# Kernel optimization log

Measured on AMD Instinct MI355X. Metric: run time of the kernel, lower is better.

The kernel has to match this reference:

```python
import jax, jax.numpy as jnp
import numpy as np

N = 50000    # nodes
E = 800000   # edges per relation
R = 3        # relations
IN, HID, OUT = 128, 128, 64


def setup_inputs() -> dict:
    key = jax.random.key(0)
    ks = jax.random.split(key, 7)
    x = jax.random.normal(ks[0], (N, IN), jnp.float32)
    src = jax.random.randint(ks[1], (R, E), 0, N)
    dst = jax.random.randint(ks[2], (R, E), 0, N)
    W1 = jax.random.normal(ks[3], (R, IN, HID), jnp.float32) / np.sqrt(IN)
    b1 = jnp.zeros((R, HID), jnp.float32)
    W2 = jax.random.normal(ks[4], (R, HID, OUT), jnp.float32) / np.sqrt(HID)
    b2 = jnp.zeros((R, OUT), jnp.float32)
    return {"x": x, "src": src, "dst": dst, "W1": W1, "b1": b1, "W2": W2, "b2": b2}


def _rel_conv(x, src, dst, W, b):
    """dgl GraphConv with norm='both' and self-loops added (dgl.add_self_loop).
    out = D_dst^{-1/2} A_sl (D_src^{-1/2} X W) + b  (weight order commutes)."""
    loop = jnp.arange(N, dtype=src.dtype)
    s = jnp.concatenate([src, loop])  # [E+N] self-loops appended
    d = jnp.concatenate([dst, loop])
    ones = jnp.ones(s.shape[0], x.dtype)
    deg_out = jax.ops.segment_sum(ones, s, num_segments=N)  # >= 1 due to self loops
    deg_in = jax.ops.segment_sum(ones, d, num_segments=N)
    h = (x * jax.lax.rsqrt(deg_out)[:, None]) @ W          # [N, F_out]
    agg = jax.ops.segment_sum(h[s], d, num_segments=N)     # gather-scatter SpMM
    return agg * jax.lax.rsqrt(deg_in)[:, None] + b


def _hetero_layer(x, src, dst, W, b):
    # HeteroGraphConv with aggregate='sum': sum per-relation GraphConv outputs.
    out = _rel_conv(x, src[0], dst[0], W[0], b[0])
    for r in range(1, R):  # small fixed relation count
        out = out + _rel_conv(x, src[r], dst[r], W[r], b[r])
    return out


def reference(x, src, dst, W1, b1, W2, b2):
    h = jax.nn.relu(_hetero_layer(x, src, dst, W1, b1))
    return _hetero_layer(h, src, dst, W2, b2)
```

## Files before the change

### kernel.cpp

```cpp
#include <hip/hip_runtime.h>
#include <hip/hip_fp16.h>


constexpr int N   = 50000;
constexpr int R   = 3;
constexpr int IN  = 128;
constexpr int HID = 128;
constexpr int OUT = 64;
constexpr int M   = R * N;
constexpr int BK  = 1024;
constexpr int NBKT = (M + BK - 1) / BK;
constexpr int CHUNK = 8192;
constexpr int KB  = 24;
constexpr int CVT_N4 = N * IN / 4;
constexpr int WPK   = 6 * KB * 64;
constexpr int WPK_B = (WPK + 255) / 256;

typedef _Float16 half8 __attribute__((ext_vector_type(8)));
typedef float floatx16 __attribute__((ext_vector_type(16)));

__global__ void prep_kernel(const float* __restrict__ x,
                            const float* __restrict__ W1, const float* __restrict__ W2,
                            const float* __restrict__ b1, const float* __restrict__ b2,
                            uint2* __restrict__ x16,
                            __half* __restrict__ F1, __half* __restrict__ F2,
                            float* __restrict__ bsum1, float* __restrict__ bsum2) {
    int b = blockIdx.x;
    if (b == 0) {
        int t = threadIdx.x;
        if (t < HID) bsum1[t] = b1[t] + b1[HID + t] + b1[2 * HID + t];
        if (t < OUT) bsum2[t] = b2[t] + b2[OUT + t] + b2[2 * OUT + t];
        return;
    }
    if (b <= WPK_B) {
        int idx = (b - 1) * 256 + threadIdx.x;
        if (idx < 4 * KB * 64) {
            int nt = idx / (KB * 64), rem = idx % (KB * 64);
            int kb = rem / 64, lane = rem % 64;
            int c = nt * 32 + (lane & 31);
            int k0 = kb * 16 + (lane >> 5) * 8;
            __half h[8];
#pragma unroll
            for (int j = 0; j < 8; j++) h[j] = __float2half_rn(W1[(k0 + j) * 128 + c]);
            *(uint4*)(F1 + (size_t)idx * 8) = *(uint4*)h;
        } else if (idx < 6 * KB * 64) {
            int i2 = idx - 4 * KB * 64;
            int nt = i2 / (KB * 64), rem = i2 % (KB * 64);
            int kb = rem / 64, lane = rem % 64;
            int c = nt * 32 + (lane & 31);
            int k0 = kb * 16 + (lane >> 5) * 8;
            __half h[8];
#pragma unroll
            for (int j = 0; j < 8; j++) h[j] = __float2half_rn(W2[(k0 + j) * 64 + c]);
            *(uint4*)(F2 + (size_t)i2 * 8) = *(uint4*)h;
        }
        return;
    }
    int i = (b - 1 - WPK_B) * 256 + threadIdx.x;
    if (i >= CVT_N4) return;
    float4 v = ((const float4*)x)[i];
    __half2 a = __floats2half2_rn(v.x, v.y);
    __half2 c = __floats2half2_rn(v.z, v.w);
    uint2 o;
    o.x = *(unsigned*)&a;
    o.y = *(unsigned*)&c;
    x16[i] = o;
}

__global__ __launch_bounds__(256) void p1_kernel(const int* __restrict__ src,
                                                 const int* __restrict__ dst,
                                                 int E, int RE, int nb,
                                                 int* __restrict__ bh) {
    __shared__ int hd[NBKT], hs[NBKT];
    for (int i = threadIdx.x; i < NBKT; i += 256) { hd[i] = 0; hs[i] = 0; }
    __syncthreads();
    int beg = blockIdx.x * CHUNK, end = min(RE, beg + CHUNK);
    for (int g = beg + (int)threadIdx.x; g < end; g += 256) {
        int rb = ((g >= E) + (g >= 2 * E)) * N;
        atomicAdd(&hd[(rb + dst[g]) >> 10], 1);
        atomicAdd(&hs[(rb + src[g]) >> 10], 1);
    }
    __syncthreads();
    for (int i = threadIdx.x; i < NBKT; i += 256) {
        bh[i * nb + blockIdx.x] = hd[i];
        bh[(NBKT + i) * nb + blockIdx.x] = hs[i];
    }
}

__global__ void scan1_kernel(const int* __restrict__ in, int* __restrict__ out,
                             int* __restrict__ partials, int L) {
    __shared__ int lds[1024];
    int t = threadIdx.x;
    int idx = blockIdx.x * 1024 + t;
    int v = (idx < L) ? in[idx] : 0;
    lds[t] = v;
    __syncthreads();
    for (int off = 1; off < 1024; off <<= 1) {
        int u = (t >= off) ? lds[t - off] : 0;
        __syncthreads();
        lds[t] += u;
        __syncthreads();
    }
    if (idx < L) out[idx] = lds[t] - v;
    if (t == 1023) partials[blockIdx.x] = lds[1023];
}

__global__ void scan2_kernel(int* __restrict__ partials, int nb1) {
    __shared__ int lds[256];
    int t = threadIdx.x;
    int v = (t < nb1) ? partials[t] : 0;
    lds[t] = v;
    __syncthreads();
    for (int off = 1; off < 256; off <<= 1) {
        int u = (t >= off) ? lds[t - off] : 0;
        __syncthreads();
        lds[t] += u;
        __syncthreads();
    }
    if (t < nb1) partials[t] = lds[t] - v;
}

__global__ __launch_bounds__(256) void p3_kernel(const int* __restrict__ src,
                                                 const int* __restrict__ dst,
                                                 int E, int RE, int nb,
                                                 const int* __restrict__ scanv,
                                                 const int* __restrict__ partials,
                                                 int* __restrict__ ebd,
                                                 unsigned short* __restrict__ ebs) {
    __shared__ int cd[NBKT], cs[NBKT];
    for (int i = threadIdx.x; i < NBKT; i += 256) {
        int id = i * nb + blockIdx.x;
        int is = (NBKT + i) * nb + blockIdx.x;
        cd[i] = scanv[id] + partials[id >> 10];
        cs[i] = scanv[is] + partials[is >> 10] - RE;
    }
    __syncthreads();
    int beg = blockIdx.x * CHUNK, end = min(RE, beg + CHUNK);
    for (int g = beg + (int)threadIdx.x; g < end; g += 256) {
        int rb = ((g >= E) + (g >= 2 * E)) * N;
        int s  = src[g];
        int kd = rb + dst[g];
        int pd = atomicAdd(&cd[kd >> 10], 1);
        ebd[pd] = (s << 10) | (kd & 1023);
        int ks = rb + s;
        int ps = atomicAdd(&cs[ks >> 10], 1);
        ebs[ps] = (unsigned short)(ks & 1023);
    }
}

__global__ __launch_bounds__(1024) void pbs_kernel(const int* __restrict__ scanv,
                                                   const int* __restrict__ partials,
                                                   int nb, int RE,
                                                   const unsigned short* __restrict__ ebs,
                                                   float* __restrict__ rs_out) {
    __shared__ int cnt[BK];
    int t = threadIdx.x;
    int k = blockIdx.x;
    int i0 = (NBKT + k) * nb;
    int segbeg = scanv[i0] + partials[i0 >> 10] - RE;
    int segend;
    if (k == NBKT - 1) segend = RE;
    else {
        int i1 = i0 + nb;
        segend = scanv[i1] + partials[i1 >> 10] - RE;
    }
    cnt[t] = 0;
    __syncthreads();
    for (int e = segbeg + t; e < segend; e += 1024)
        atomicAdd(&cnt[(int)ebs[e]], 1);
    __syncthreads();
    int slot = k * BK + t;
    if (slot < M) rs_out[slot] = rsqrtf((float)(cnt[t] + 1));
}

__global__ __launch_bounds__(1024) void pbd_kernel(const int* __restrict__ scanv,
                                                   const int* __restrict__ partials,
                                                   int nb, int RE,
                                                   const int* __restrict__ ebd,
                                                   const float* __restrict__ rs_out,
                                                   int* __restrict__ row_ptr,
                                                   float* __restrict__ rs_in,
                                                   unsigned int* __restrict__ esrc) {
    __shared__ int cnt[BK];
    __shared__ int cur[BK];
    int t = threadIdx.x;
    int k = blockIdx.x;
    int i0 = k * nb;
    int segbeg = scanv[i0] + partials[i0 >> 10];
    int segend;
    if (k == NBKT - 1) segend = RE;
    else {
        int i1 = (k + 1) * nb;
        segend = scanv[i1] + partials[i1 >> 10];
    }
    cnt[t] = 0;
    __syncthreads();
    for (int e = segbeg + t; e < segend; e += 1024)
        atomicAdd(&cnt[ebd[e] & 1023], 1);
    __syncthreads();
    int slot = k * BK + t;
    int c = cnt[t];
    cur[t] = c;
    __syncthreads();
    for (int off = 1; off < 1024; off <<= 1) {
        int u = (t >= off) ? cur[t - off] : 0;
        __syncthreads();
        cur[t] += u;
        __syncthreads();
    }
    int excl = cur[t] - c;
    if (slot < M) {
        row_ptr[slot] = segbeg + excl;
        rs_in[slot] = rsqrtf((float)(c + 1));
    }
    if (k == NBKT - 1 && t == 0) row_ptr[M] = RE;
    __syncthreads();
    cur[t] = segbeg + excl;
    __syncthreads();
    for (int e = segbeg + t; e < segend; e += 1024) {
        int v = ebd[e];
        int key = k * BK + (v & 1023);
        int r = (key >= 2 * N) + (key >= N);
        unsigned s = (unsigned)(v >> 10);
        int pos = atomicAdd(&cur[v & 1023], 1);
        __half h = __float2half_rn(rs_out[r * N + s]);
        esrc[pos] = s | ((unsigned)__half_as_ushort(h) << 16);
    }
}

__global__ __launch_bounds__(256) void gather_kernel(const __half* __restrict__ Xh,
                                                     const float* __restrict__ rs_in,
                                                     const float* __restrict__ rs_out,
                                                     const int* __restrict__ row_ptr,
                                                     const unsigned int* __restrict__ esrc,
                                                     __half* __restrict__ Z16) {
    int n = blockIdx.x * 4 + (threadIdx.x >> 6);
    if (n >= N) return;
    int lane = threadIdx.x & 63;
    int g = lane >> 4;
    int cl = lane & 15;
    const __half* xrow = Xh + (long)n * 128 + cl * 8;
    uint4 xn = *(const uint4*)xrow;
#pragma unroll
    for (int r = 0; r < R; r++) {
        int key = r * N + n;
        int beg = row_ptr[key], end = row_ptr[key + 1];
        __half2 a0 = __float2half2_rn(0.f), a1 = a0, a2 = a0, a3 = a0;
        for (int e = beg; e < end; e += 24) {
            unsigned u[6];
#pragma unroll
            for (int j = 0; j < 6; j++) {
                int idx = e + 4 * j + g;
                u[j] = (idx < end) ? esrc[idx] : 0u;
            }
            uint4 y[6];
#pragma unroll
            for (int j = 0; j < 6; j++)
                y[j] = *(const uint4*)(Xh + (long)(u[j] & 0xffffu) * 128 + cl * 8);
#pragma unroll
            for (int j = 0; j < 6; j++) {
                __half2 cj = __half2half2(__ushort_as_half((unsigned short)(u[j] >> 16)));
                a0 = __hfma2(*(__half2*)&y[j].x, cj, a0);
                a1 = __hfma2(*(__half2*)&y[j].y, cj, a1);
                a2 = __hfma2(*(__half2*)&y[j].z, cj, a2);
                a3 = __hfma2(*(__half2*)&y[j].w, cj, a3);
            }
        }
#pragma unroll
        for (int off = 16; off < 64; off <<= 1) {
            unsigned w0 = *(unsigned*)&a0, w1 = *(unsigned*)&a1;
            unsigned w2 = *(unsigned*)&a2, w3 = *(unsigned*)&a3;
            unsigned v0 = (unsigned)__shfl_xor((int)w0, off, 64);
            unsigned v1 = (unsigned)__shfl_xor((int)w1, off, 64);
            unsigned v2 = (unsigned)__shfl_xor((int)w2, off, 64);
            unsigned v3 = (unsigned)__shfl_xor((int)w3, off, 64);
            a0 = __hadd2(a0, *(__half2*)&v0);
            a1 = __hadd2(a1, *(__half2*)&v1);
            a2 = __hadd2(a2, *(__half2*)&v2);
            a3 = __hadd2(a3, *(__half2*)&v3);
        }
        __half2 cs = __float2half2_rn(rs_out[key]);
        a0 = __hfma2(*(__half2*)&xn.x, cs, a0);
        a1 = __hfma2(*(__half2*)&xn.y, cs, a1);
        a2 = __hfma2(*(__half2*)&xn.z, cs, a2);
        a3 = __hfma2(*(__half2*)&xn.w, cs, a3);
        __half2 ri = __float2half2_rn(rs_in[key]);
        a0 = __hmul2(a0, ri);
        a1 = __hmul2(a1, ri);
        a2 = __hmul2(a2, ri);
        a3 = __hmul2(a3, ri);
        if (g == 0) {
            uint4 o;
            o.x = *(unsigned*)&a0;
            o.y = *(unsigned*)&a1;
            o.z = *(unsigned*)&a2;
            o.w = *(unsigned*)&a3;
            *(uint4*)(Z16 + (long)n * 384 + r * 128 + cl * 8) = o;
        }
    }
}

__global__ __launch_bounds__(256) void mfma_gemm1_kernel(const __half* __restrict__ Z16,
                                                         const __half* __restrict__ F,
                                                         const float* __restrict__ bias,
                                                         __half* __restrict__ H16) {
    int wave = threadIdx.x >> 6, lane = threadIdx.x & 63;
    int m0 = blockIdx.x * 128 + wave * 32;
    int mr = min(m0 + (lane & 31), N - 1);
    const half8* A = (const half8*)(Z16 + (long)mr * 384 + (lane >> 5) * 8);
    const half8* B = (const half8*)F;
    floatx16 acc[4];
#pragma unroll
    for (int i = 0; i < 4; i++)
#pragma unroll
        for (int j = 0; j < 16; j++) acc[i][j] = 0.f;

    half8 a = A[0];
    for (int kb = 0; kb < KB; kb++) {
        half8 an = (kb < KB - 1) ? A[(kb + 1) * 2] : a;
#pragma unroll
        for (int nt = 0; nt < 4; nt++) {
            half8 b = B[(nt * KB + kb) * 64 + lane];
            acc[nt] = __builtin_amdgcn_mfma_f32_32x32x16_f16(a, b, acc[nt], 0, 0, 0);
        }
        a = an;
    }
    float bv[4];
#pragma unroll
    for (int nt = 0; nt < 4; nt++) bv[nt] = bias[nt * 32 + (lane & 31)];
    int rbase = m0 + 4 * (lane >> 5);
    int col0 = lane & 31;
#pragma unroll
    for (int nt = 0; nt < 4; nt++) {
#pragma unroll
        for (int reg = 0; reg < 16; reg++) {
            int row = rbase + (reg & 3) + 8 * (reg >> 2);
            if (row < N) {
                float v = fmaxf(acc[nt][reg] + bv[nt], 0.f);
                H16[(long)row * 128 + nt * 32 + col0] = __float2half_rn(v);
            }
        }
    }
}

__global__ __launch_bounds__(256) void mfma_gemmY_kernel(const __half* __restrict__ H16,
                                                         const __half* __restrict__ F,
                                                         __half* __restrict__ Y2) {
    int wave = threadIdx.x >> 6, lane = threadIdx.x & 63;
    int r = blockIdx.y;
    int m0 = blockIdx.x * 128 + wave * 32;
    int mr = min(m0 + (lane & 31), N - 1);
    const half8* A = (const half8*)(H16 + (long)mr * 128 + (lane >> 5) * 8);
    const half8* B = (const half8*)F;
    floatx16 acc[2];
#pragma unroll
    for (int i = 0; i < 2; i++)
#pragma unroll
        for (int j = 0; j < 16; j++) acc[i][j] = 0.f;

#pragma unroll
    for (int kbr = 0; kbr < 8; kbr++) {
        half8 a = A[kbr * 2];
#pragma unroll
        for (int nt = 0; nt < 2; nt++) {
            half8 b = B[(nt * KB + r * 8 + kbr) * 64 + lane];
            acc[nt] = __builtin_amdgcn_mfma_f32_32x32x16_f16(a, b, acc[nt], 0, 0, 0);
        }
    }
    int rbase = m0 + 4 * (lane >> 5);
    int col0 = lane & 31;
    __half* Yr = Y2 + (long)r * N * 64;
#pragma unroll
    for (int nt = 0; nt < 2; nt++) {
#pragma unroll
        for (int reg = 0; reg < 16; reg++) {
            int row = rbase + (reg & 3) + 8 * (reg >> 2);
            if (row < N)
                Yr[(long)row * 64 + nt * 32 + col0] = __float2half_rn(acc[nt][reg]);
        }
    }
}

__global__ __launch_bounds__(256) void gather_out_kernel(const __half* __restrict__ Y2,
                                                         const float* __restrict__ rs_in,
                                                         const float* __restrict__ rs_out,
                                                         const int* __restrict__ row_ptr,
                                                         const unsigned int* __restrict__ esrc,
                                                         const float* __restrict__ bias,
                                                         float* __restrict__ outp) {
    int n = blockIdx.x * 4 + (threadIdx.x >> 6);
    if (n >= N) return;
    int lane = threadIdx.x & 63;
    int g = lane >> 4;
    int cl = lane & 15;
    float4 tot = ((const float4*)bias)[cl];
#pragma unroll
    for (int r = 0; r < R; r++) {
        int key = r * N + n;
        const __half* Yr = Y2 + (long)r * N * 64;
        __half2 a0 = __float2half2_rn(0.f), a1 = a0;
        int beg = row_ptr[key], end = row_ptr[key + 1];
        for (int e = beg; e < end; e += 32) {
            unsigned u[8];
#pragma unroll
            for (int j = 0; j < 8; j++) {
                int idx = e + 4 * j + g;
                u[j] = (idx < end) ? esrc[idx] : 0u;
            }
            uint2 y[8];
#pragma unroll
            for (int j = 0; j < 8; j++)
                y[j] = *(const uint2*)(Yr + (long)(u[j] & 0xffffu) * 64 + cl * 4);
#pragma unroll
            for (int j = 0; j < 8; j++) {
                __half2 cj = __half2half2(__ushort_as_half((unsigned short)(u[j] >> 16)));
                a0 = __hfma2(*(__half2*)&y[j].x, cj, a0);
                a1 = __hfma2(*(__half2*)&y[j].y, cj, a1);
            }
        }
#pragma unroll
        for (int off = 16; off < 64; off <<= 1) {
            unsigned w0 = *(unsigned*)&a0, w1 = *(unsigned*)&a1;
            unsigned v0 = (unsigned)__shfl_xor((int)w0, off, 64);
            unsigned v1 = (unsigned)__shfl_xor((int)w1, off, 64);
            a0 = __hadd2(a0, *(__half2*)&v0);
            a1 = __hadd2(a1, *(__half2*)&v1);
        }
        uint2 ys = *(const uint2*)(Yr + (long)n * 64 + cl * 4);
        __half2 cs = __float2half2_rn(rs_out[key]);
        a0 = __hfma2(*(__half2*)&ys.x, cs, a0);
        a1 = __hfma2(*(__half2*)&ys.y, cs, a1);
        float2 f0 = __half22float2(a0);
        float2 f1 = __half22float2(a1);
        float ri = rs_in[key];
        tot.x += ri * f0.x;
        tot.y += ri * f0.y;
        tot.z += ri * f1.x;
        tot.w += ri * f1.y;
    }
    if (g == 0) *(float4*)(outp + (long)n * 64 + cl * 4) = tot;
}

extern "C" void kernel_launch(void* const* d_in, const int* in_sizes, int n_in,
                              void* d_out, int out_size, void* d_ws, size_t ws_size,
                              hipStream_t stream) {
    const float* x  = (const float*)d_in[0];
    const int*  src = (const int*)d_in[1];
    const int*  dst = (const int*)d_in[2];
    const float* W1 = (const float*)d_in[3];
    const float* b1 = (const float*)d_in[4];
    const float* W2 = (const float*)d_in[5];
    const float* b2 = (const float*)d_in[6];
    float* out = (float*)d_out;
    const int E  = in_sizes[1] / R;
    const int RE = in_sizes[1];
    const int nb = (RE + CHUNK - 1) / CHUNK;
    const int L  = 2 * NBKT * nb;
    const int nb1 = (L + 1023) / 1024;

    char* ws = (char*)d_ws;
    size_t off = 0;
    auto alloc = [&](size_t bytes) -> void* {
        void* p = ws + off;
        off += (bytes + 255) & ~(size_t)255;
        return p;
    };
    float* bsum1    = (float*)alloc(HID * 4);
    float* bsum2    = (float*)alloc(OUT * 4);
    float* rs_in    = (float*)alloc((size_t)M * 4);
    float* rs_out   = (float*)alloc((size_t)M * 4);
    int*   row_ptr  = (int*)alloc((size_t)(M + 1) * 4);
    int*   bh       = (int*)alloc((size_t)L * 4);
    int*   scanv    = (int*)alloc((size_t)L * 4);
    int*   partials = (int*)alloc((size_t)nb1 * 4);
    unsigned* esrc  = (unsigned*)alloc((size_t)RE * 4);
    __half* F1      = (__half*)alloc((size_t)4 * KB * 64 * 8 * 2);
    __half* F2      = (__half*)alloc((size_t)2 * KB * 64 * 8 * 2);
    char*  regA     = (char*)alloc((size_t)N * 384 * 2);
    int*   ebd      = (int*)regA;
    unsigned short* ebs = (unsigned short*)(regA + (size_t)RE * 4);
    __half* Z16     = (__half*)regA;
    __half* Y2      = (__half*)regA;
    __half* x16     = (__half*)alloc((size_t)N * IN * 2);
    __half* H16     = (__half*)alloc((size_t)N * HID * 2);

    prep_kernel<<<1 + WPK_B + (CVT_N4 + 255) / 256, 256, 0, stream>>>(
        x, W1, W2, b1, b2, (uint2*)x16, F1, F2, bsum1, bsum2);
    p1_kernel<<<nb, 256, 0, stream>>>(src, dst, E, RE, nb, bh);
    scan1_kernel<<<nb1, 1024, 0, stream>>>(bh, scanv, partials, L);
    scan2_kernel<<<1, 256, 0, stream>>>(partials, nb1);
    p3_kernel<<<nb, 256, 0, stream>>>(src, dst, E, RE, nb, scanv, partials, ebd, ebs);
    pbs_kernel<<<NBKT, 1024, 0, stream>>>(scanv, partials, nb, RE, ebs, rs_out);
    pbd_kernel<<<NBKT, 1024, 0, stream>>>(scanv, partials, nb, RE, ebd, rs_out,
                                          row_ptr, rs_in, esrc);

    const int ab  = (N + 3) / 4;
    const int ggb = (N + 127) / 128;

    gather_kernel<<<ab, 256, 0, stream>>>(x16, rs_in, rs_out, row_ptr, esrc, Z16);
    mfma_gemm1_kernel<<<ggb, 256, 0, stream>>>(Z16, F1, bsum1, H16);
    mfma_gemmY_kernel<<<dim3(ggb, R), 256, 0, stream>>>(H16, F2, Y2);
    gather_out_kernel<<<ab, 256, 0, stream>>>(Y2, rs_in, rs_out, row_ptr, esrc,
                                              bsum2, out);
}
```

Baseline: 347.6 us.

## Compute out-degrees with global atomics instead of bucketed source sort

Source-side out-degree counting moves off the bucket histogram, scatter and per-bucket count path onto direct global atomicAdd into a deg_out array. That array is zeroed in the prep kernel, and rs_out is computed in a fused scan2 kernel. This removes the ebs scatter, the pbs_kernel launch and half of the histogram and scan work. In exchange it takes 2.4M global atomics to random addresses, which can contend and add L2 traffic.

```diff
diff --git a/kernel.cpp b/kernel.cpp
--- a/kernel.cpp
+++ b/kernel.cpp
@@ -15,6 +15,7 @@
 constexpr int CVT_N4 = N * IN / 4;
 constexpr int WPK   = 6 * KB * 64;
 constexpr int WPK_B = (WPK + 255) / 256;
+constexpr int RSB   = (M + 255) / 256;
 
 typedef _Float16 half8 __attribute__((ext_vector_type(8)));
 typedef float floatx16 __attribute__((ext_vector_type(16)));
@@ -24,7 +25,8 @@
                             const float* __restrict__ b1, const float* __restrict__ b2,
                             uint2* __restrict__ x16,
                             __half* __restrict__ F1, __half* __restrict__ F2,
-                            float* __restrict__ bsum1, float* __restrict__ bsum2) {
+                            float* __restrict__ bsum1, float* __restrict__ bsum2,
+                            int* __restrict__ deg_out) {
     int b = blockIdx.x;
     if (b == 0) {
         int t = threadIdx.x;
@@ -56,7 +58,12 @@
         }
         return;
     }
-    int i = (b - 1 - WPK_B) * 256 + threadIdx.x;
+    if (b <= WPK_B + RSB) {
+        int i = (b - 1 - WPK_B) * 256 + threadIdx.x;
+        if (i < M) deg_out[i] = 0;
+        return;
+    }
+    int i = (b - 1 - WPK_B - RSB) * 256 + threadIdx.x;
     if (i >= CVT_N4) return;
     float4 v = ((const float4*)x)[i];
     __half2 a = __floats2half2_rn(v.x, v.y);
@@ -70,21 +77,20 @@
 __global__ __launch_bounds__(256) void p1_kernel(const int* __restrict__ src,
                                                  const int* __restrict__ dst,
                                                  int E, int RE, int nb,
-                                                 int* __restrict__ bh) {
-    __shared__ int hd[NBKT], hs[NBKT];
-    for (int i = threadIdx.x; i < NBKT; i += 256) { hd[i] = 0; hs[i] = 0; }
+                                                 int* __restrict__ bh,
+                                                 int* __restrict__ deg_out) {
+    __shared__ int hd[NBKT];
+    for (int i = threadIdx.x; i < NBKT; i += 256) hd[i] = 0;
     __syncthreads();
     int beg = blockIdx.x * CHUNK, end = min(RE, beg + CHUNK);
     for (int g = beg + (int)threadIdx.x; g < end; g += 256) {
         int rb = ((g >= E) + (g >= 2 * E)) * N;
         atomicAdd(&hd[(rb + dst[g]) >> 10], 1);
-        atomicAdd(&hs[(rb + src[g]) >> 10], 1);
-    }
-    __syncthreads();
-    for (int i = threadIdx.x; i < NBKT; i += 256) {
+        atomicAdd(&deg_out[rb + src[g]], 1);
+    }
+    __syncthreads();
+    for (int i = threadIdx.x; i < NBKT; i += 256)
         bh[i * nb + blockIdx.x] = hd[i];
-        bh[(NBKT + i) * nb + blockIdx.x] = hs[i];
-    }
 }
 
 __global__ void scan1_kernel(const int* __restrict__ in, int* __restrict__ out,
@@ -105,19 +111,26 @@
     if (t == 1023) partials[blockIdx.x] = lds[1023];
 }
 
-__global__ void scan2_kernel(int* __restrict__ partials, int nb1) {
-    __shared__ int lds[256];
-    int t = threadIdx.x;
-    int v = (t < nb1) ? partials[t] : 0;
-    lds[t] = v;
-    __syncthreads();
-    for (int off = 1; off < 256; off <<= 1) {
-        int u = (t >= off) ? lds[t - off] : 0;
+__global__ void scan2_rs_kernel(int* __restrict__ partials, int nb1,
+                                const int* __restrict__ deg_out,
+                                float* __restrict__ rs_out) {
+    if (blockIdx.x == 0) {
+        __shared__ int lds[256];
+        int t = threadIdx.x;
+        int v = (t < nb1) ? partials[t] : 0;
+        lds[t] = v;
         __syncthreads();
-        lds[t] += u;
-        __syncthreads();
-    }
-    if (t < nb1) partials[t] = lds[t] - v;
+        for (int off = 1; off < 256; off <<= 1) {
+            int u = (t >= off) ? lds[t - off] : 0;
+            __syncthreads();
+            lds[t] += u;
+            __syncthreads();
+        }
+        if (t < nb1) partials[t] = lds[t] - v;
+        return;
+    }
+    int i = (blockIdx.x - 1) * 256 + threadIdx.x;
+    if (i < M) rs_out[i] = rsqrtf((float)(deg_out[i] + 1));
 }
 
 __global__ __launch_bounds__(256) void p3_kernel(const int* __restrict__ src,
@@ -125,14 +138,11 @@
                                                  int E, int RE, int nb,
                                                  const int* __restrict__ scanv,
                                                  const int* __restrict__ partials,
-                                                 int* __restrict__ ebd,
-                                                 unsigned short* __restrict__ ebs) {
-    __shared__ int cd[NBKT], cs[NBKT];
+                                                 int* __restrict__ ebd) {
+    __shared__ int cd[NBKT];
     for (int i = threadIdx.x; i < NBKT; i += 256) {
         int id = i * nb + blockIdx.x;
-        int is = (NBKT + i) * nb + blockIdx.x;
         cd[i] = scanv[id] + partials[id >> 10];
-        cs[i] = scanv[is] + partials[is >> 10] - RE;
     }
     __syncthreads();
     int beg = blockIdx.x * CHUNK, end = min(RE, beg + CHUNK);
@@ -142,35 +152,7 @@
         int kd = rb + dst[g];
         int pd = atomicAdd(&cd[kd >> 10], 1);
         ebd[pd] = (s << 10) | (kd & 1023);
-        int ks = rb + s;
-        int ps = atomicAdd(&cs[ks >> 10], 1);
-        ebs[ps] = (unsigned short)(ks & 1023);
-    }
-}
-
-__global__ __launch_bounds__(1024) void pbs_kernel(const int* __restrict__ scanv,
-                                                   const int* __restrict__ partials,
-                                                   int nb, int RE,
-                                                   const unsigned short* __restrict__ ebs,
-                                                   float* __restrict__ rs_out) {
-    __shared__ int cnt[BK];
-    int t = threadIdx.x;
-    int k = blockIdx.x;
-    int i0 = (NBKT + k) * nb;
-    int segbeg = scanv[i0] + partials[i0 >> 10] - RE;
-    int segend;
-    if (k == NBKT - 1) segend = RE;
-    else {
-        int i1 = i0 + nb;
-        segend = scanv[i1] + partials[i1 >> 10] - RE;
-    }
-    cnt[t] = 0;
-    __syncthreads();
-    for (int e = segbeg + t; e < segend; e += 1024)
-        atomicAdd(&cnt[(int)ebs[e]], 1);
-    __syncthreads();
-    int slot = k * BK + t;
-    if (slot < M) rs_out[slot] = rsqrtf((float)(cnt[t] + 1));
+    }
 }
 
 __global__ __launch_bounds__(1024) void pbd_kernel(const int* __restrict__ scanv,
@@ -455,7 +437,7 @@
     const int E  = in_sizes[1] / R;
     const int RE = in_sizes[1];
     const int nb = (RE + CHUNK - 1) / CHUNK;
-    const int L  = 2 * NBKT * nb;
+    const int L  = NBKT * nb;
     const int nb1 = (L + 1023) / 1024;
 
     char* ws = (char*)d_ws;
@@ -469,6 +451,7 @@
     float* bsum2    = (float*)alloc(OUT * 4);
     float* rs_in    = (float*)alloc((size_t)M * 4);
     float* rs_out   = (float*)alloc((size_t)M * 4);
+    int*   deg_out  = (int*)alloc((size_t)M * 4);
     int*   row_ptr  = (int*)alloc((size_t)(M + 1) * 4);
     int*   bh       = (int*)alloc((size_t)L * 4);
     int*   scanv    = (int*)alloc((size_t)L * 4);
@@ -478,19 +461,17 @@
     __half* F2      = (__half*)alloc((size_t)2 * KB * 64 * 8 * 2);
     char*  regA     = (char*)alloc((size_t)N * 384 * 2);
     int*   ebd      = (int*)regA;
-    unsigned short* ebs = (unsigned short*)(regA + (size_t)RE * 4);
     __half* Z16     = (__half*)regA;
     __half* Y2      = (__half*)regA;
     __half* x16     = (__half*)alloc((size_t)N * IN * 2);
     __half* H16     = (__half*)alloc((size_t)N * HID * 2);
 
-    prep_kernel<<<1 + WPK_B + (CVT_N4 + 255) / 256, 256, 0, stream>>>(
-        x, W1, W2, b1, b2, (uint2*)x16, F1, F2, bsum1, bsum2);
-    p1_kernel<<<nb, 256, 0, stream>>>(src, dst, E, RE, nb, bh);
+    prep_kernel<<<1 + WPK_B + RSB + (CVT_N4 + 255) / 256, 256, 0, stream>>>(
+        x, W1, W2, b1, b2, (uint2*)x16, F1, F2, bsum1, bsum2, deg_out);
+    p1_kernel<<<nb, 256, 0, stream>>>(src, dst, E, RE, nb, bh, deg_out);
     scan1_kernel<<<nb1, 1024, 0, stream>>>(bh, scanv, partials, L);
-    scan2_kernel<<<1, 256, 0, stream>>>(partials, nb1);
-    p3_kernel<<<nb, 256, 0, stream>>>(src, dst, E, RE, nb, scanv, partials, ebd, ebs);
-    pbs_kernel<<<NBKT, 1024, 0, stream>>>(scanv, partials, nb, RE, ebs, rs_out);
+    scan2_rs_kernel<<<1 + RSB, 256, 0, stream>>>(partials, nb1, deg_out, rs_out);
+    p3_kernel<<<nb, 256, 0, stream>>>(src, dst, E, RE, nb, scanv, partials, ebd);
     pbd_kernel<<<NBKT, 1024, 0, stream>>>(scanv, partials, nb, RE, ebd, rs_out,
                                           row_ptr, rs_in, esrc);
 
```

Result: slower. 413.7 us (+19.0%).
